# Performance work log

Hardware: AMD Instinct MI355X
Metric: run time of the kernel (lower is better)

## Reference

```python
import jax, jax.numpy as jnp
import numpy as np

N_NODES = 100000


def _glorot(key, shape):
    fan_in, fan_out = shape[1], shape[0]
    lim = np.sqrt(6.0 / (fan_in + fan_out))
    return jax.random.uniform(key, shape, jnp.float32, -lim, lim)


def setup_inputs() -> dict:
    key = jax.random.key(0)
    ks = jax.random.split(key, 12)
    x = jax.random.normal(ks[0], (N_NODES, 64), jnp.float32)
    edge_index = jax.random.randint(ks[1], (2, 1600000), 0, N_NODES, jnp.int64)
    return {
        "x": x,
        "edge_index": edge_index,
        # SAGEConv layer 1: lin_l (neighbors, with bias), lin_r (root, no bias)
        "W1l": _glorot(ks[2], (64, 64)), "b1": jnp.zeros((64,), jnp.float32), "W1r": _glorot(ks[3], (64, 64)),
        "W2l": _glorot(ks[4], (64, 64)), "b2": jnp.zeros((64,), jnp.float32), "W2r": _glorot(ks[5], (64, 64)),
        "W3l": _glorot(ks[6], (32, 64)), "b3": jnp.zeros((32,), jnp.float32), "W3r": _glorot(ks[7], (32, 64)),
        "Wreg": _glorot(ks[8], (1, 32)), "breg": jnp.zeros((1,), jnp.float32),
    }


def _sage_conv(x, src, dst, Wl, b, Wr):
    # mean aggregation of source-node features at destination nodes
    msg_sum = jax.ops.segment_sum(x[src], dst, num_segments=N_NODES)  # [N, d]
    deg = jax.ops.segment_sum(jnp.ones_like(src, dtype=x.dtype), dst, num_segments=N_NODES)
    mean = msg_sum / jnp.maximum(deg, 1.0)[:, None]
    return mean @ Wl.T + b + x @ Wr.T


def reference(x, edge_index, W1l, b1, W1r, W2l, b2, W2r, W3l, b3, W3r, Wreg, breg):
    src, dst = edge_index[0], edge_index[1]
    h = jax.nn.relu(_sage_conv(x, src, dst, W1l, b1, W1r))
    h = jax.nn.relu(_sage_conv(h, src, dst, W2l, b2, W2r))
    h = jax.nn.relu(_sage_conv(h, src, dst, W3l, b3, W3r))
    return (h @ Wreg.T + breg).squeeze(-1)  # [N]
```

## Files before the change

kernel.cpp:

```cpp
#include <hip/hip_runtime.h>
#include <math.h>

#define N_NODES 100000
#define N_EDGES 1600000
#define NB 782
#define NTILES 6250

typedef unsigned int uint;
typedef __attribute__((ext_vector_type(8))) short bf16x8;
typedef __attribute__((ext_vector_type(4))) float f32x4;

__device__ inline ushort f2bf(float f) {
    uint u = __float_as_uint(f);
    uint r = (u + 0x7fffu + ((u >> 16) & 1u)) >> 16;
    return (ushort)r;
}
__device__ inline uint pack2bf(float lo, float hi) {
    return (uint)f2bf(lo) | ((uint)f2bf(hi) << 16);
}

__global__ void cast_bf16(const float* __restrict__ in, ushort* __restrict__ out, int n4) {
    int i = blockIdx.x * blockDim.x + threadIdx.x;
    if (i < n4) {
        float4 v = ((const float4*)in)[i];
        uint2 o;
        o.x = pack2bf(v.x, v.y);
        o.y = pack2bf(v.z, v.w);
        ((uint2*)out)[i] = o;
    }
}

__global__ void prep_wfrag(const float* __restrict__ W1l, const float* __restrict__ W1r,
                           const float* __restrict__ W2l, const float* __restrict__ W2r,
                           const float* __restrict__ W3l, const float* __restrict__ W3r,
                           ushort* __restrict__ wf) {
    int idx = blockIdx.x * 256 + threadIdx.x;
    if (idx >= 20480) return;
    const float *Wl, *Wr;
    int base, KT;
    if (idx < 8192)       { base = 0;     Wl = W1l; Wr = W1r; KT = 128; }
    else if (idx < 16384) { base = 8192;  Wl = W2l; Wr = W2r; KT = 128; }
    else if (idx < 18432) { base = 16384; Wl = W3l; Wr = 0;   KT = 64; }
    else                  { base = 18432; Wl = W3r; Wr = 0;   KT = 64; }
    int r = idx - base;
    int f = r >> 9;
    int l = (r >> 3) & 63;
    int i = r & 7;
    int nks = KT >> 5;
    int nt = f / nks, ks = f - nt * nks;
    int k = ks * 32 + ((l >> 4) << 3) + i;
    int j = nt * 16 + (l & 15);
    float v = (k < 64) ? Wl[j * 64 + k] : Wr[j * 64 + (k - 64)];
    wf[idx] = f2bf(v);
}

__global__ void bucket_hist(const int* __restrict__ dst, int* __restrict__ bucketCnt, int nE) {
    __shared__ int hist[NB];
    const int PER = (N_EDGES + 255) / 256;
    int e0 = blockIdx.x * PER;
    int e1 = min(e0 + PER, nE);
    for (int i = threadIdx.x; i < NB; i += 1024) hist[i] = 0;
    __syncthreads();
    for (int e = e0 + threadIdx.x; e < e1; e += 1024)
        atomicAdd(&hist[dst[e] >> 7], 1);
    __syncthreads();
    for (int i = threadIdx.x; i < NB; i += 1024) {
        int c = hist[i];
        if (c) atomicAdd(&bucketCnt[i], c);
    }
}

__global__ void scan_buckets(const int* __restrict__ bucketCnt, int* __restrict__ bucketBase,
                             int* __restrict__ cursor) {
    __shared__ int s[1024];
    int tid = threadIdx.x;
    int v = (tid < NB) ? bucketCnt[tid] : 0;
    s[tid] = v;
    __syncthreads();
    for (int off = 1; off < 1024; off <<= 1) {
        int t = (tid >= off) ? s[tid - off] : 0;
        __syncthreads();
        s[tid] += t;
        __syncthreads();
    }
    if (tid < NB) {
        int excl = s[tid] - v;
        bucketBase[tid] = excl;
        cursor[tid] = excl;
    }
    if (tid == 0) bucketBase[NB] = s[NB - 1];
}

__global__ void partition_kernel(const int* __restrict__ src, const int* __restrict__ dst,
                                 int* __restrict__ cursor, int* __restrict__ part, int nE) {
    __shared__ int hist[NB];
    __shared__ int base[NB];
    __shared__ int rank[NB];
    const int PER = (N_EDGES + 255) / 256;
    int e0 = blockIdx.x * PER;
    int e1 = min(e0 + PER, nE);
    for (int i = threadIdx.x; i < NB; i += 1024) { hist[i] = 0; rank[i] = 0; }
    __syncthreads();
    for (int e = e0 + threadIdx.x; e < e1; e += 1024)
        atomicAdd(&hist[dst[e] >> 7], 1);
    __syncthreads();
    for (int i = threadIdx.x; i < NB; i += 1024) {
        int c = hist[i];
        base[i] = c ? atomicAdd(&cursor[i], c) : 0;
    }
    __syncthreads();
    for (int e = e0 + threadIdx.x; e < e1; e += 1024) {
        int d = dst[e];
        int bk = d >> 7;
        int r = atomicAdd(&rank[bk], 1);
        part[base[bk] + r] = src[e] | ((d & 127) << 20);
    }
}

__global__ void bucket_fill2(const int* __restrict__ bucketBase, const int* __restrict__ part,
                             int* __restrict__ col, int* __restrict__ rowptr,
                             float* __restrict__ invdeg, int n) {
    __shared__ int cnt[128];
    __shared__ int cnt2[128];
    __shared__ int exclS[128];
    __shared__ int s[128];
    int b = blockIdx.x;
    int d0 = b << 7;
    int dl = min(128, n - d0);
    int ebeg = bucketBase[b], eend = bucketBase[b + 1];
    if (threadIdx.x < 128) { cnt[threadIdx.x] = 0; cnt2[threadIdx.x] = 0; }
    __syncthreads();
    for (int i = ebeg + (int)threadIdx.x; i < eend; i += 512)
        atomicAdd(&cnt[part[i] >> 20], 1);
    __syncthreads();
    if (threadIdx.x < 128) s[threadIdx.x] = cnt[threadIdx.x];
    __syncthreads();
    for (int off = 1; off < 128; off <<= 1) {
        int t = 0;
        if (threadIdx.x < 128 && threadIdx.x >= (unsigned)off) t = s[threadIdx.x - off];
        __syncthreads();
        if (threadIdx.x < 128) s[threadIdx.x] += t;
        __syncthreads();
    }
    if ((int)threadIdx.x < dl) {
        int c = cnt[threadIdx.x];
        int ex = ebeg + s[threadIdx.x] - c;
        rowptr[d0 + threadIdx.x] = ex;
        invdeg[d0 + threadIdx.x] = 1.0f / fmaxf((float)c, 1.0f);
        exclS[threadIdx.x] = ex;
    }
    if (threadIdx.x == 0 && d0 + dl == n) rowptr[n] = eend;
    __syncthreads();
    for (int i = ebeg + (int)threadIdx.x; i < eend; i += 512) {
        int v = part[i];
        int doff = v >> 20;
        int pos = exclS[doff] + atomicAdd(&cnt2[doff], 1);
        col[pos] = v & 0xFFFFF;
    }
}

__global__ void gather_mean(const ushort* __restrict__ xb, const int* __restrict__ rowptr,
                            const int* __restrict__ col, const float* __restrict__ invdeg,
                            ushort* __restrict__ meanb, int n) {
    int tid = blockIdx.x * blockDim.x + threadIdx.x;
    int wid = tid >> 6;
    int lane = threadIdx.x & 63;
    int grp = lane >> 3;
    int li = lane & 7;
    int node = wid * 8 + grp;
    if (node >= n) return;
    int beg = rowptr[node];
    int end = rowptr[node + 1];
    int fb = li * 8;
    float a0 = 0.f, a1 = 0.f, a2 = 0.f, a3 = 0.f, a4 = 0.f, a5 = 0.f, a6 = 0.f, a7 = 0.f;
    for (int i = beg; i < end; i += 8) {
        int idx = i + li;
        int ci = (idx < end) ? col[idx] : 0;
        int cnt = end - i;
#pragma unroll
        for (int t = 0; t < 8; ++t) {
            if (t < cnt) {
                int s = __shfl(ci, grp * 8 + t, 64);
                uint4 w = *(const uint4*)(xb + (size_t)s * 64 + fb);
                a0 += __uint_as_float(w.x << 16);
                a1 += __uint_as_float(w.x & 0xffff0000u);
                a2 += __uint_as_float(w.y << 16);
                a3 += __uint_as_float(w.y & 0xffff0000u);
                a4 += __uint_as_float(w.z << 16);
                a5 += __uint_as_float(w.z & 0xffff0000u);
                a6 += __uint_as_float(w.w << 16);
                a7 += __uint_as_float(w.w & 0xffff0000u);
            }
        }
    }
    float id = invdeg[node];
    uint4 o;
    o.x = pack2bf(a0 * id, a1 * id);
    o.y = pack2bf(a2 * id, a3 * id);
    o.z = pack2bf(a4 * id, a5 * id);
    o.w = pack2bf(a6 * id, a7 * id);
    *(uint4*)(meanb + (size_t)node * 64 + fb) = o;
}

__global__ void gather_mean32(const ushort* __restrict__ gb, const int* __restrict__ rowptr,
                              const int* __restrict__ col, const float* __restrict__ invdeg,
                              ushort* __restrict__ mean32b, int n) {
    int tid = blockIdx.x * blockDim.x + threadIdx.x;
    int wid = tid >> 6;
    int lane = threadIdx.x & 63;
    int grp = lane >> 2;
    int li = lane & 3;
    int node = wid * 16 + grp;
    if (node >= n) return;
    int beg = rowptr[node];
    int end = rowptr[node + 1];
    int fb = li * 8;
    float a0 = 0.f, a1 = 0.f, a2 = 0.f, a3 = 0.f, a4 = 0.f, a5 = 0.f, a6 = 0.f, a7 = 0.f;
    for (int i = beg; i < end; i += 4) {
        int idx = i + li;
        int ci = (idx < end) ? col[idx] : 0;
        int cnt = end - i;
#pragma unroll
        for (int t = 0; t < 4; ++t) {
            if (t < cnt) {
                int s = __shfl(ci, grp * 4 + t, 64);
                uint4 w = *(const uint4*)(gb + (size_t)s * 32 + fb);
                a0 += __uint_as_float(w.x << 16);
                a1 += __uint_as_float(w.x & 0xffff0000u);
                a2 += __uint_as_float(w.y << 16);
                a3 += __uint_as_float(w.y & 0xffff0000u);
                a4 += __uint_as_float(w.z << 16);
                a5 += __uint_as_float(w.z & 0xffff0000u);
                a6 += __uint_as_float(w.w << 16);
                a7 += __uint_as_float(w.w & 0xffff0000u);
            }
        }
    }
    float id = invdeg[node];
    uint4 o;
    o.x = pack2bf(a0 * id, a1 * id);
    o.y = pack2bf(a2 * id, a3 * id);
    o.z = pack2bf(a4 * id, a5 * id);
    o.w = pack2bf(a6 * id, a7 * id);
    *(uint4*)(mean32b + (size_t)node * 32 + fb) = o;
}

__global__ void __launch_bounds__(256)
mfma_transform(const ushort* __restrict__ rootb, const ushort* __restrict__ meanb,
               const ushort* __restrict__ wfrag, const float* __restrict__ bias,
               ushort* __restrict__ outb, int ntiles) {
    int wave = threadIdx.x >> 6;
    int lane = threadIdx.x & 63;

    bf16x8 wf[4][4];
#pragma unroll
    for (int nt = 0; nt < 4; ++nt)
#pragma unroll
        for (int ks = 0; ks < 4; ++ks)
            wf[nt][ks] = *(const bf16x8*)(wfrag + (size_t)((nt * 4 + ks) * 64 + lane) * 8);

    float bl[4];
#pragma unroll
    for (int nt = 0; nt < 4; ++nt) bl[nt] = bias[nt * 16 + (lane & 15)];

    int arow = lane & 15;
    int koff = (lane >> 4) * 8;
    int crow = (lane >> 4) * 4;
    int nwaves = gridDim.x * 4;

    for (int tile = blockIdx.x * 4 + wave; tile < ntiles; tile += nwaves) {
        int n0 = tile * 16;
        const ushort* mrow = meanb + (size_t)(n0 + arow) * 64 + koff;
        const ushort* xrow = rootb + (size_t)(n0 + arow) * 64 + koff;
        bf16x8 a0 = *(const bf16x8*)(mrow);
        bf16x8 a1 = *(const bf16x8*)(mrow + 32);
        bf16x8 a2 = *(const bf16x8*)(xrow);
        bf16x8 a3 = *(const bf16x8*)(xrow + 32);
#pragma unroll
        for (int nt = 0; nt < 4; ++nt) {
            f32x4 c = {0.f, 0.f, 0.f, 0.f};
            c = __builtin_amdgcn_mfma_f32_16x16x32_bf16(a0, wf[nt][0], c, 0, 0, 0);
            c = __builtin_amdgcn_mfma_f32_16x16x32_bf16(a1, wf[nt][1], c, 0, 0, 0);
            c = __builtin_amdgcn_mfma_f32_16x16x32_bf16(a2, wf[nt][2], c, 0, 0, 0);
            c = __builtin_amdgcn_mfma_f32_16x16x32_bf16(a3, wf[nt][3], c, 0, 0, 0);
#pragma unroll
            for (int i = 0; i < 4; ++i) {
                float v = fmaxf(c[i] + bl[nt], 0.0f);
                outb[(size_t)(n0 + crow + i) * 64 + nt * 16 + (lane & 15)] = f2bf(v);
            }
        }
    }
}

__global__ void __launch_bounds__(256)
mfma_pretrans3(const ushort* __restrict__ hb, const ushort* __restrict__ wfrag,
               ushort* __restrict__ gb, int ntiles) {
    int wave = threadIdx.x >> 6;
    int lane = threadIdx.x & 63;

    bf16x8 wf[2][2];
#pragma unroll
    for (int nt = 0; nt < 2; ++nt)
#pragma unroll
        for (int ks = 0; ks < 2; ++ks)
            wf[nt][ks] = *(const bf16x8*)(wfrag + (size_t)((nt * 2 + ks) * 64 + lane) * 8);

    int arow = lane & 15;
    int koff = (lane >> 4) * 8;
    int crow = (lane >> 4) * 4;
    int nwaves = gridDim.x * 4;

    for (int tile = blockIdx.x * 4 + wave; tile < ntiles; tile += nwaves) {
        int n0 = tile * 16;
        const ushort* hrow = hb + (size_t)(n0 + arow) * 64 + koff;
        bf16x8 a0 = *(const bf16x8*)(hrow);
        bf16x8 a1 = *(const bf16x8*)(hrow + 32);
#pragma unroll
        for (int nt = 0; nt < 2; ++nt) {
            f32x4 c = {0.f, 0.f, 0.f, 0.f};
            c = __builtin_amdgcn_mfma_f32_16x16x32_bf16(a0, wf[nt][0], c, 0, 0, 0);
            c = __builtin_amdgcn_mfma_f32_16x16x32_bf16(a1, wf[nt][1], c, 0, 0, 0);
#pragma unroll
            for (int i = 0; i < 4; ++i)
                gb[(size_t)(n0 + crow + i) * 32 + nt * 16 + (lane & 15)] = f2bf(c[i]);
        }
    }
}

__global__ void __launch_bounds__(256)
mfma_t3(const ushort* __restrict__ hb, const ushort* __restrict__ mean32b,
        const ushort* __restrict__ wfrag, const float* __restrict__ b3,
        const float* __restrict__ Wreg, const float* __restrict__ breg,
        float* __restrict__ out, int ntiles) {
    int wave = threadIdx.x >> 6;
    int lane = threadIdx.x & 63;

    bf16x8 wf[2][2];
#pragma unroll
    for (int nt = 0; nt < 2; ++nt)
#pragma unroll
        for (int ks = 0; ks < 2; ++ks)
            wf[nt][ks] = *(const bf16x8*)(wfrag + (size_t)((nt * 2 + ks) * 64 + lane) * 8);

    float bl[2], wr[2];
#pragma unroll
    for (int nt = 0; nt < 2; ++nt) {
        bl[nt] = b3[nt * 16 + (lane & 15)];
        wr[nt] = Wreg[nt * 16 + (lane & 15)];
    }
    float br = breg[0];

    int arow = lane & 15;
    int koff = (lane >> 4) * 8;
    int crow = (lane >> 4) * 4;
    int nwaves = gridDim.x * 4;

    for (int tile = blockIdx.x * 4 + wave; tile < ntiles; tile += nwaves) {
        int n0 = tile * 16;
        const ushort* hrow = hb + (size_t)(n0 + arow) * 64 + koff;
        bf16x8 a0 = *(const bf16x8*)(hrow);
        bf16x8 a1 = *(const bf16x8*)(hrow + 32);
        float part0 = 0.f, part1 = 0.f, part2 = 0.f, part3 = 0.f;
#pragma unroll
        for (int nt = 0; nt < 2; ++nt) {
            f32x4 c = {0.f, 0.f, 0.f, 0.f};
            c = __builtin_amdgcn_mfma_f32_16x16x32_bf16(a0, wf[nt][0], c, 0, 0, 0);
            c = __builtin_amdgcn_mfma_f32_16x16x32_bf16(a1, wf[nt][1], c, 0, 0, 0);
#pragma unroll
            for (int i = 0; i < 4; ++i) {
                ushort mw = mean32b[(size_t)(n0 + crow + i) * 32 + nt * 16 + (lane & 15)];
                float m = __uint_as_float((uint)mw << 16);
                float v = fmaxf(c[i] + bl[nt] + m, 0.0f) * wr[nt];
                if (i == 0) part0 += v;
                else if (i == 1) part1 += v;
                else if (i == 2) part2 += v;
                else part3 += v;
            }
        }
#pragma unroll
        for (int s = 1; s < 16; s <<= 1) {
            part0 += __shfl_xor(part0, s, 64);
            part1 += __shfl_xor(part1, s, 64);
            part2 += __shfl_xor(part2, s, 64);
            part3 += __shfl_xor(part3, s, 64);
        }
        if ((lane & 15) == 0) {
            float4 o;
            o.x = part0 + br; o.y = part1 + br; o.z = part2 + br; o.w = part3 + br;
            *(float4*)(out + n0 + crow) = o;
        }
    }
}

extern "C" void kernel_launch(void* const* d_in, const int* in_sizes, int n_in,
                              void* d_out, int out_size, void* d_ws, size_t ws_size,
                              hipStream_t stream) {
    const float* x    = (const float*)d_in[0];
    const int*   ei   = (const int*)d_in[1];
    const float* W1l  = (const float*)d_in[2];
    const float* b1   = (const float*)d_in[3];
    const float* W1r  = (const float*)d_in[4];
    const float* W2l  = (const float*)d_in[5];
    const float* b2   = (const float*)d_in[6];
    const float* W2r  = (const float*)d_in[7];
    const float* W3l  = (const float*)d_in[8];
    const float* b3   = (const float*)d_in[9];
    const float* W3r  = (const float*)d_in[10];
    const float* Wreg = (const float*)d_in[11];
    const float* breg = (const float*)d_in[12];

    const int* src = ei;
    const int* dst = ei + N_EDGES;

    char* p = (char*)d_ws;
    auto alloc = [&](size_t bytes) {
        char* r = p;
        p += (bytes + 255) & ~(size_t)255;
        return r;
    };
    int*    bucketCnt = (int*)alloc(NB * sizeof(int));
    int*    bucketBase= (int*)alloc((NB + 1) * sizeof(int));
    int*    cursor    = (int*)alloc(NB * sizeof(int));
    int*    rowptr    = (int*)alloc((N_NODES + 1) * sizeof(int));
    int*    col       = (int*)alloc((size_t)N_EDGES * sizeof(int));
    float*  invdeg    = (float*)alloc(N_NODES * sizeof(float));
    ushort* wfrag     = (ushort*)alloc(20480 * sizeof(ushort));
    char*   slot   = (char*)alloc((size_t)N_NODES * 64 * sizeof(ushort));
    int*    part   = (int*)slot;
    ushort* xb     = (ushort*)slot;
    ushort* gb     = (ushort*)slot;
    ushort* meanb  = (ushort*)alloc((size_t)N_NODES * 64 * sizeof(ushort));
    ushort* mean32b= meanb;
    ushort* hb     = (ushort*)alloc((size_t)N_NODES * 64 * sizeof(ushort));
    float*  out    = (float*)d_out;

    const int TB = 256;
    int castBlocks   = ((N_NODES * 64 / 4) + TB - 1) / TB;
    int g64Blocks    = (N_NODES * 8 + TB - 1) / TB;
    int g32Blocks    = (N_NODES * 4 + TB - 1) / TB;
    const int mfmaBlocks = 512;

    prep_wfrag<<<80, 256, 0, stream>>>(W1l, W1r, W2l, W2r, W3l, W3r, wfrag);
    hipMemsetAsync(bucketCnt, 0, NB * sizeof(int), stream);
    bucket_hist<<<256, 1024, 0, stream>>>(dst, bucketCnt, N_EDGES);
    scan_buckets<<<1, 1024, 0, stream>>>(bucketCnt, bucketBase, cursor);
    partition_kernel<<<256, 1024, 0, stream>>>(src, dst, cursor, part, N_EDGES);
    bucket_fill2<<<NB, 512, 0, stream>>>(bucketBase, part, col, rowptr, invdeg, N_NODES);
    cast_bf16<<<castBlocks, TB, 0, stream>>>(x, xb, N_NODES * 64 / 4);

    gather_mean<<<g64Blocks, 256, 0, stream>>>(xb, rowptr, col, invdeg, meanb, N_NODES);
    mfma_transform<<<mfmaBlocks, 256, 0, stream>>>(xb, meanb, wfrag + 0, b1, hb, NTILES);

    gather_mean<<<g64Blocks, 256, 0, stream>>>(hb, rowptr, col, invdeg, meanb, N_NODES);
    mfma_transform<<<mfmaBlocks, 256, 0, stream>>>(hb, meanb, wfrag + 8192, b2, hb, NTILES);

    mfma_pretrans3<<<mfmaBlocks, 256, 0, stream>>>(hb, wfrag + 16384, gb, NTILES);
    gather_mean32<<<g32Blocks, 256, 0, stream>>>(gb, rowptr, col, invdeg, mean32b, N_NODES);
    mfma_t3<<<mfmaBlocks, 256, 0, stream>>>(hb, mean32b, wfrag + 18432, b3, Wreg, breg, out, NTILES);
}
```

Baseline: 179.9 us.

## Fuse prep kernels, replace bucket atomics with per-block histogram scan

Merges weight-fragment prep and the x-to-bf16 cast into one launch and drops the memset. Bucket histograms are now written per partition block to a 2D table, and the scan kernel computes per-block base offsets. This removes the second histogram pass and the global atomics from the partition kernel. It also raises the MFMA grid from 512 to 1563 blocks. The trade-off is a serial scan in which each thread loops over 256 partitions, and xb now needs its own buffer.

```diff
diff --git a/kernel.cpp b/kernel.cpp
--- a/kernel.cpp
+++ b/kernel.cpp
@@ -5,6 +5,7 @@
 #define N_EDGES 1600000
 #define NB 782
 #define NTILES 6250
+#define NPART 256
 
 typedef unsigned int uint;
 typedef __attribute__((ext_vector_type(8))) short bf16x8;
@@ -19,44 +20,46 @@
     return (uint)f2bf(lo) | ((uint)f2bf(hi) << 16);
 }
 
-__global__ void cast_bf16(const float* __restrict__ in, ushort* __restrict__ out, int n4) {
-    int i = blockIdx.x * blockDim.x + threadIdx.x;
-    if (i < n4) {
-        float4 v = ((const float4*)in)[i];
-        uint2 o;
-        o.x = pack2bf(v.x, v.y);
-        o.y = pack2bf(v.z, v.w);
-        ((uint2*)out)[i] = o;
-    }
-}
-
-__global__ void prep_wfrag(const float* __restrict__ W1l, const float* __restrict__ W1r,
-                           const float* __restrict__ W2l, const float* __restrict__ W2r,
-                           const float* __restrict__ W3l, const float* __restrict__ W3r,
-                           ushort* __restrict__ wf) {
-    int idx = blockIdx.x * 256 + threadIdx.x;
-    if (idx >= 20480) return;
-    const float *Wl, *Wr;
-    int base, KT;
-    if (idx < 8192)       { base = 0;     Wl = W1l; Wr = W1r; KT = 128; }
-    else if (idx < 16384) { base = 8192;  Wl = W2l; Wr = W2r; KT = 128; }
-    else if (idx < 18432) { base = 16384; Wl = W3l; Wr = 0;   KT = 64; }
-    else                  { base = 18432; Wl = W3r; Wr = 0;   KT = 64; }
-    int r = idx - base;
-    int f = r >> 9;
-    int l = (r >> 3) & 63;
-    int i = r & 7;
-    int nks = KT >> 5;
-    int nt = f / nks, ks = f - nt * nks;
-    int k = ks * 32 + ((l >> 4) << 3) + i;
-    int j = nt * 16 + (l & 15);
-    float v = (k < 64) ? Wl[j * 64 + k] : Wr[j * 64 + (k - 64)];
-    wf[idx] = f2bf(v);
-}
-
-__global__ void bucket_hist(const int* __restrict__ dst, int* __restrict__ bucketCnt, int nE) {
+__global__ void misc_kernel(const float* __restrict__ W1l, const float* __restrict__ W1r,
+                            const float* __restrict__ W2l, const float* __restrict__ W2r,
+                            const float* __restrict__ W3l, const float* __restrict__ W3r,
+                            ushort* __restrict__ wf,
+                            const float* __restrict__ x, ushort* __restrict__ xb) {
+    if (blockIdx.x < 80) {
+        int idx = blockIdx.x * 256 + threadIdx.x;
+        if (idx >= 20480) return;
+        const float *Wl, *Wr;
+        int base, KT;
+        if (idx < 8192)       { base = 0;     Wl = W1l; Wr = W1r; KT = 128; }
+        else if (idx < 16384) { base = 8192;  Wl = W2l; Wr = W2r; KT = 128; }
+        else if (idx < 18432) { base = 16384; Wl = W3l; Wr = 0;   KT = 64; }
+        else                  { base = 18432; Wl = W3r; Wr = 0;   KT = 64; }
+        int r = idx - base;
+        int f = r >> 9;
+        int l = (r >> 3) & 63;
+        int i = r & 7;
+        int nks = KT >> 5;
+        int nt = f / nks, ks = f - nt * nks;
+        int k = ks * 32 + ((l >> 4) << 3) + i;
+        int j = nt * 16 + (l & 15);
+        float v = (k < 64) ? Wl[j * 64 + k] : Wr[j * 64 + (k - 64)];
+        wf[idx] = f2bf(v);
+    } else {
+        const int n4 = N_NODES * 64 / 4;
+        int i0 = (blockIdx.x - 80) * 256 + threadIdx.x;
+        for (int i = i0; i < n4; i += 400 * 256) {
+            float4 v = ((const float4*)x)[i];
+            uint2 o;
+            o.x = pack2bf(v.x, v.y);
+            o.y = pack2bf(v.z, v.w);
+            ((uint2*)xb)[i] = o;
+        }
+    }
+}
+
+__global__ void bucket_hist(const int* __restrict__ dst, int* __restrict__ hist2D, int nE) {
     __shared__ int hist[NB];
-    const int PER = (N_EDGES + 255) / 256;
+    const int PER = (N_EDGES + NPART - 1) / NPART;
     int e0 = blockIdx.x * PER;
     int e1 = min(e0 + PER, nE);
     for (int i = threadIdx.x; i < NB; i += 1024) hist[i] = 0;
@@ -64,18 +67,18 @@
     for (int e = e0 + threadIdx.x; e < e1; e += 1024)
         atomicAdd(&hist[dst[e] >> 7], 1);
     __syncthreads();
-    for (int i = threadIdx.x; i < NB; i += 1024) {
-        int c = hist[i];
-        if (c) atomicAdd(&bucketCnt[i], c);
-    }
-}
-
-__global__ void scan_buckets(const int* __restrict__ bucketCnt, int* __restrict__ bucketBase,
-                             int* __restrict__ cursor) {
+    for (int i = threadIdx.x; i < NB; i += 1024)
+        hist2D[blockIdx.x * NB + i] = hist[i];
+}
+
+__global__ void scan_buckets(const int* __restrict__ hist2D, int* __restrict__ bucketBase,
+                             int* __restrict__ base2D) {
     __shared__ int s[1024];
     int tid = threadIdx.x;
-    int v = (tid < NB) ? bucketCnt[tid] : 0;
-    s[tid] = v;
+    int tot = 0;
+    if (tid < NB)
+        for (int b = 0; b < NPART; ++b) tot += hist2D[b * NB + tid];
+    s[tid] = tot;
     __syncthreads();
     for (int off = 1; off < 1024; off <<= 1) {
         int t = (tid >= off) ? s[tid - off] : 0;
@@ -84,29 +87,26 @@
         __syncthreads();
     }
     if (tid < NB) {
-        int excl = s[tid] - v;
-        bucketBase[tid] = excl;
-        cursor[tid] = excl;
+        int run = s[tid] - tot;
+        bucketBase[tid] = run;
+        for (int b = 0; b < NPART; ++b) {
+            base2D[b * NB + tid] = run;
+            run += hist2D[b * NB + tid];
+        }
     }
     if (tid == 0) bucketBase[NB] = s[NB - 1];
 }
 
 __global__ void partition_kernel(const int* __restrict__ src, const int* __restrict__ dst,
-                                 int* __restrict__ cursor, int* __restrict__ part, int nE) {
-    __shared__ int hist[NB];
+                                 const int* __restrict__ base2D, int* __restrict__ part, int nE) {
     __shared__ int base[NB];
     __shared__ int rank[NB];
-    const int PER = (N_EDGES + 255) / 256;
+    const int PER = (N_EDGES + NPART - 1) / NPART;
     int e0 = blockIdx.x * PER;
     int e1 = min(e0 + PER, nE);
-    for (int i = threadIdx.x; i < NB; i += 1024) { hist[i] = 0; rank[i] = 0; }
-    __syncthreads();
-    for (int e = e0 + threadIdx.x; e < e1; e += 1024)
-        atomicAdd(&hist[dst[e] >> 7], 1);
-    __syncthreads();
     for (int i = threadIdx.x; i < NB; i += 1024) {
-        int c = hist[i];
-        base[i] = c ? atomicAdd(&cursor[i], c) : 0;
+        base[i] = base2D[blockIdx.x * NB + i];
+        rank[i] = 0;
     }
     __syncthreads();
     for (int e = e0 + threadIdx.x; e < e1; e += 1024) {
@@ -418,35 +418,32 @@
         p += (bytes + 255) & ~(size_t)255;
         return r;
     };
-    int*    bucketCnt = (int*)alloc(NB * sizeof(int));
+    int*    hist2D    = (int*)alloc((size_t)NPART * NB * sizeof(int));
+    int*    base2D    = (int*)alloc((size_t)NPART * NB * sizeof(int));
     int*    bucketBase= (int*)alloc((NB + 1) * sizeof(int));
-    int*    cursor    = (int*)alloc(NB * sizeof(int));
     int*    rowptr    = (int*)alloc((N_NODES + 1) * sizeof(int));
     int*    col       = (int*)alloc((size_t)N_EDGES * sizeof(int));
     float*  invdeg    = (float*)alloc(N_NODES * sizeof(float));
     ushort* wfrag     = (ushort*)alloc(20480 * sizeof(ushort));
-    char*   slot   = (char*)alloc((size_t)N_NODES * 64 * sizeof(ushort));
+    char*   slot   = (char*)alloc((size_t)N_EDGES * sizeof(int));
     int*    part   = (int*)slot;
-    ushort* xb     = (ushort*)slot;
     ushort* gb     = (ushort*)slot;
+    ushort* xb     = (ushort*)alloc((size_t)N_NODES * 64 * sizeof(ushort));
     ushort* meanb  = (ushort*)alloc((size_t)N_NODES * 64 * sizeof(ushort));
     ushort* mean32b= meanb;
     ushort* hb     = (ushort*)alloc((size_t)N_NODES * 64 * sizeof(ushort));
     float*  out    = (float*)d_out;
 
     const int TB = 256;
-    int castBlocks   = ((N_NODES * 64 / 4) + TB - 1) / TB;
     int g64Blocks    = (N_NODES * 8 + TB - 1) / TB;
     int g32Blocks    = (N_NODES * 4 + TB - 1) / TB;
-    const int mfmaBlocks = 512;
-
-    prep_wfrag<<<80, 256, 0, stream>>>(W1l, W1r, W2l, W2r, W3l, W3r, wfrag);
-    hipMemsetAsync(bucketCnt, 0, NB * sizeof(int), stream);
-    bucket_hist<<<256, 1024, 0, stream>>>(dst, bucketCnt, N_EDGES);
-    scan_buckets<<<1, 1024, 0, stream>>>(bucketCnt, bucketBase, cursor);
-    partition_kernel<<<256, 1024, 0, stream>>>(src, dst, cursor, part, N_EDGES);
+    const int mfmaBlocks = 1563;
+
+    misc_kernel<<<480, 256, 0, stream>>>(W1l, W1r, W2l, W2r, W3l, W3r, wfrag, x, xb);
+    bucket_hist<<<NPART, 1024, 0, stream>>>(dst, hist2D, N_EDGES);
+    scan_buckets<<<1, 1024, 0, stream>>>(hist2D, bucketBase, base2D);
+    partition_kernel<<<NPART, 1024, 0, stream>>>(src, dst, base2D, part, N_EDGES);
     bucket_fill2<<<NB, 512, 0, stream>>>(bucketBase, part, col, rowptr, invdeg, N_NODES);
-    cast_bf16<<<castBlocks, TB, 0, stream>>>(x, xb, N_NODES * 64 / 4);
 
     gather_mean<<<g64Blocks, 256, 0, stream>>>(xb, rowptr, col, invdeg, meanb, N_NODES);
     mfma_transform<<<mfmaBlocks, 256, 0, stream>>>(xb, meanb, wfrag + 0, b1, hb, NTILES);
```

New measurement: 196.8 us. +9.4%, slower.
